# Kernel tuning notes

Measured on AMD Instinct MI355X. Metric: run time of the kernel, lower is better.

## Reference

```python
import jax, jax.numpy as jnp
import numpy as np

B, S, D, A = 8, 4096, 128, 128


def _pos_encoding(seq_len, dim):
    # sin/cos positional encoding, same construction as the torch buffer
    pos = np.arange(seq_len, dtype=np.float32)[:, None]
    div = np.exp(np.arange(0, dim, 2, dtype=np.float32) * (-np.log(10000.0) / dim))
    pe = np.zeros((seq_len, dim), dtype=np.float32)
    pe[:, 0::2] = np.sin(pos * div)
    pe[:, 1::2] = np.cos(pos * div)
    return jnp.asarray(pe)


def setup_inputs() -> dict:
    key = jax.random.key(0)
    ks = jax.random.split(key, 7)
    sc = 1.0 / np.sqrt(D)
    return {
        "x": jax.random.normal(ks[0], (B, S, D), dtype=jnp.float32),
        "Wq": jax.random.normal(ks[1], (D, A), dtype=jnp.float32) * sc,
        "bq": jnp.zeros((A,), dtype=jnp.float32),
        "Wk": jax.random.normal(ks[2], (D, A), dtype=jnp.float32) * sc,
        "bk": jnp.zeros((A,), dtype=jnp.float32),
        "Wv": jax.random.normal(ks[3], (D, A), dtype=jnp.float32) * sc,
        "bv": jnp.zeros((A,), dtype=jnp.float32),
    }


def reference(x, Wq, bq, Wk, bk, Wv, bv):
    b, s, d = x.shape
    pe = _pos_encoding(s, d)  # [S, D]
    xp = x + pe[None]  # broadcast add of positional encoding
    q = xp @ Wq + bq  # [B, S, A]
    k = xp @ Wk + bk
    v = xp @ Wv + bv
    scale = 1.0 / jnp.sqrt(jnp.asarray(Wq.shape[1], dtype=jnp.float32))
    scores = jnp.einsum("bsa,bta->bst", q, k) * scale  # [B, S, S]
    weights = jax.nn.softmax(scores, axis=-1)
    out = jnp.einsum("bst,bta->bsa", weights, v)  # [B, S, A]
    return out
```

## Files before the change

kernel.cpp:

```cpp
#include <hip/hip_runtime.h>

#define BB 8
#define SS 4096
#define DD 128

typedef __attribute__((ext_vector_type(8))) short v8s;
typedef __attribute__((ext_vector_type(4))) float v4f;
typedef __attribute__((ext_vector_type(16))) float v16f;

__device__ __forceinline__ unsigned short f2bf(float f) {
    unsigned int u = __float_as_uint(f);
    u += 0x7fffu + ((u >> 16) & 1u);
    return (unsigned short)(u >> 16);
}
__device__ __forceinline__ unsigned int pk_bf16(float a, float b) {
    unsigned int ua = __float_as_uint(a) + 0x8000u;
    unsigned int ub = __float_as_uint(b) + 0x8000u;
    return __builtin_amdgcn_perm(ub, ua, 0x07060302u);
}

#if !defined(__HIP_DEVICE_COMPILE__)
#define MFMA16(a, b, c) (c)
#define MFMA32(a, b, c) (c)
#define GLDS16(g, l)
#define WAITVM(n)
#define WAITLGKM()
#define BAR()
#else
#define MFMA16(a, b, c) __builtin_amdgcn_mfma_f32_16x16x32_bf16((a), (b), (c), 0, 0, 0)
#define MFMA32(a, b, c) __builtin_amdgcn_mfma_f32_32x32x16_bf16((a), (b), (c), 0, 0, 0)
#define GLDS16(g, l)                                                         \
    __builtin_amdgcn_global_load_lds(                                        \
        (const __attribute__((address_space(1))) unsigned int*)(g),          \
        (__attribute__((address_space(3))) unsigned int*)(l), 16, 0, 0)
#define WAITVM(n) asm volatile("s_waitcnt vmcnt(" #n ")" ::: "memory")
#define WAITLGKM() asm volatile("s_waitcnt lgkmcnt(0)" ::: "memory")
#define BAR()                                                                \
    do {                                                                     \
        asm volatile("" ::: "memory");                                       \
        __builtin_amdgcn_s_barrier();                                        \
        __builtin_amdgcn_sched_barrier(0);                                   \
        asm volatile("" ::: "memory");                                       \
    } while (0)
#endif

#if !defined(__HIP_DEVICE_COMPILE__)
#define EXP2F(x) exp2f(x)
#elif __has_builtin(__builtin_amdgcn_exp2f)
#define EXP2F(x) __builtin_amdgcn_exp2f(x)
#else
#define EXP2F(x) exp2f(x)
#endif

#define QSCALE 0.12751743f

__global__ __launch_bounds__(256) void prep_kernel(
    const float* __restrict__ Wq, const float* __restrict__ Wk,
    const float* __restrict__ Wv, unsigned short* __restrict__ Wt)
{
    int id = blockIdx.x * 256 + threadIdx.x;
    int w = id >> 14;
    int n = (id >> 7) & 127;
    int k = id & 127;
    const float* W = (w == 0) ? Wq : (w == 1) ? Wk : Wv;
    Wt[id] = f2bf(W[k * 128 + n]);
}

__global__ __launch_bounds__(256, 2) void proj_kernel(
    const float* __restrict__ x, const unsigned short* __restrict__ Wt,
    const float* __restrict__ bq, const float* __restrict__ bk,
    const float* __restrict__ bv,
    unsigned short* __restrict__ qo, unsigned short* __restrict__ ko,
    unsigned short* __restrict__ vF)
{
    __shared__ __attribute__((aligned(16))) unsigned short w_lds[128 * 136];
    __shared__ __attribute__((aligned(16))) unsigned short o_lds[9216];

    const int tid = threadIdx.x;
    const int wave = tid >> 6;
    const int lane = tid & 63;
    const int quad = lane >> 4;
    const int l15 = lane & 15;
    const int rbase = blockIdx.x * 64;

    const int flatrow = rbase + wave * 16 + l15;
    const int srow = flatrow & 4095;
    v8s af[4];
#pragma unroll
    for (int kc = 0; kc < 4; ++kc) {
        const int kbase = kc * 32 + quad * 8;
        const v4f* xp = (const v4f*)(x + (size_t)flatrow * DD + kbase);
        v4f x0 = xp[0], x1 = xp[1];
        float p[8];
#pragma unroll
        for (int j = 0; j < 8; j += 2) {
            float freq = __expf((float)(kbase + j) * -0.07195578415606394f);
            float arg = (float)srow * freq;
            p[j] = __sinf(arg);
            p[j + 1] = __cosf(arg);
        }
        v8s a;
#pragma unroll
        for (int j = 0; j < 4; ++j) a[j] = (short)f2bf(x0[j] + p[j]);
#pragma unroll
        for (int j = 0; j < 4; ++j) a[4 + j] = (short)f2bf(x1[j] + p[4 + j]);
        af[kc] = a;
    }

    const int quadp = ((quad & 1) << 1) | (quad >> 1);
    const int b0 = rbase >> 12, s0 = rbase & 4095;
    const size_t t0 = (size_t)b0 * 128 + (s0 >> 5);

#pragma unroll 1
    for (int m = 0; m < 3; ++m) {
        const float* bias = (m == 0) ? bq : (m == 1) ? bk : bv;
        __syncthreads();
        const unsigned short* Wp = Wt + (m << 14);
#pragma unroll
        for (int it = 0; it < 8; ++it) {
            int id = it * 256 + tid;
            int n = id >> 4, c8 = id & 15;
            *(v8s*)(w_lds + n * 136 + c8 * 8) = *(const v8s*)(Wp + n * 128 + c8 * 8);
        }
        __syncthreads();

#pragma unroll
        for (int nb = 0; nb < 8; ++nb) {
            const int col = nb * 16 + l15;
            v4f acc = {0.f, 0.f, 0.f, 0.f};
#pragma unroll
            for (int kc = 0; kc < 4; ++kc) {
                v8s bf = *(const v8s*)(w_lds + col * 136 + kc * 32 + quad * 8);
                acc = MFMA16(af[kc], bf, acc);
            }
            float bval = bias[col];
#pragma unroll
            for (int reg = 0; reg < 4; ++reg) {
                float val = acc[reg] + bval;
                if (m == 0) {
                    int lr = wave * 16 + quad * 4 + reg;
                    o_lds[lr * 136 + col] = f2bf(val * QSCALE);
                } else if (m == 1) {
                    int lr = wave * 16 + quad * 4 + reg;
                    o_lds[lr * 136 + col] = f2bf(val);
                } else {
                    int plr = wave * 16 + quadp * 4 + reg;
                    o_lds[col * 72 + plr] = f2bf(val);
                }
            }
        }
        __syncthreads();

        if (m <= 1) {
            unsigned short* outp = (m == 0) ? qo : ko;
#pragma unroll
            for (int it = 0; it < 4; ++it) {
                int id = it * 256 + tid;
                int r = id >> 4, c8 = id & 15;
                *(v8s*)(outp + (size_t)(rbase + r) * DD + c8 * 8) =
                    *(const v8s*)(o_lds + r * 136 + c8 * 8);
            }
        } else {
#pragma unroll
            for (int it = 0; it < 4; ++it) {
                int id = it * 256 + tid;
                int c = id >> 7, col = id & 127;
                *(v8s*)(vF + (((t0 + (c >> 2)) * 4 + (c & 3)) * 128 + col) * 8) =
                    *(const v8s*)(o_lds + col * 72 + c * 8);
            }
        }
    }
}

#define HKEYS 2048
#define NT 32
__global__ __launch_bounds__(512, 2) void flash_kernel(
    const unsigned short* __restrict__ qp,
    const unsigned short* __restrict__ kp,
    const unsigned short* __restrict__ vF,
    float* __restrict__ outp)
{
    __shared__ __attribute__((aligned(16))) unsigned short k_lds[2][2][8192];
    __shared__ float xl[8][32];

    const int tid = threadIdx.x;
    const int wave = tid >> 6;
    const int lane = tid & 63;
    const int hi = lane >> 5;
    const int l31 = lane & 31;
    const int half = wave >> 2;
    const int qs = wave & 3;
    const int wv = wave & 3;
    const int bid = blockIdx.x;
    const int b = bid & 7;
    const int qt = bid >> 3;
    const int qbase = qt * 128;

    const size_t qrow = (size_t)(b * SS + qbase + qs * 32 + l31) * DD;
    v8s qf[8];
#pragma unroll
    for (int kc = 0; kc < 8; ++kc)
        qf[kc] = *(const v8s*)(qp + qrow + kc * 16 + hi * 8);

    v16f o[4];
#pragma unroll
    for (int fg = 0; fg < 4; ++fg)
#pragma unroll
        for (int r = 0; r < 16; ++r) o[fg][r] = 0.f;
    float lp = 0.f;

    const int kro = half * 32768 + l31 * 256 + ((hi ^ (l31 & 15)) << 4);

    const int krow = wv * 4 + (lane >> 4);
    const unsigned short* ksrc =
        kp + ((size_t)(b * SS + half * HKEYS) + krow) * DD +
        (((lane & 15) ^ krow) << 3);
    unsigned short* kd0 = &k_lds[half][0][wv * 512];

    const size_t tbase = ((size_t)(b * 128 + half * 64)) * 4096;
    const unsigned short* vW = vF + tbase + hi * 1024 + l31 * 8;

    v8s X[8], Y[8];
    auto stage = [&](int p, int t) {
        unsigned short* kd = kd0 + p * 8192;
        const unsigned short* ks = ksrc + (size_t)t * 64 * DD;
#pragma unroll
        for (int it = 0; it < 4; ++it)
            GLDS16(ks + (size_t)it * 16 * DD, kd + it * 2048);
    };
    auto loadV = [&](v8s (&buf)[8], int u) {
        const unsigned short* p = vW + (size_t)u * 4096;
#pragma unroll
        for (int g = 0; g < 2; ++g)
#pragma unroll
            for (int fg = 0; fg < 4; ++fg)
                buf[g * 4 + fg] = *(const v8s*)(p + g * 2048 + fg * 256);
    };
    auto compute = [&](int p, int sub, const v8s (&buf)[8]) {
        const int ka = kro + p * 16384 + sub * 8192;
        v16f s;
#pragma unroll
        for (int r = 0; r < 16; ++r) s[r] = 0.f;
#pragma unroll
        for (int kc = 0; kc < 8; ++kc) {
            v8s af = *(const v8s*)((const char*)k_lds + (ka ^ (kc << 5)));
            s = MFMA32(af, qf[kc], s);
        }
        float e[16];
#pragma unroll
        for (int r = 0; r < 16; ++r) e[r] = EXP2F(s[r]);
        lp += (((e[0] + e[1]) + (e[2] + e[3])) + ((e[4] + e[5]) + (e[6] + e[7]))) +
              (((e[8] + e[9]) + (e[10] + e[11])) + ((e[12] + e[13]) + (e[14] + e[15])));
        union { v8s v[2]; unsigned int u[8]; } P;
#pragma unroll
        for (int g = 0; g < 2; ++g)
#pragma unroll
            for (int m = 0; m < 4; ++m)
                P.u[g * 4 + m] = pk_bf16(e[2 * m + 8 * g], e[2 * m + 8 * g + 1]);
#pragma unroll
        for (int g = 0; g < 2; ++g)
#pragma unroll
            for (int fg = 0; fg < 4; ++fg)
                o[fg] = MFMA32(P.v[g], buf[g * 4 + fg], o[fg]);
    };

    stage(0, 0);
    loadV(X, 0);
    loadV(Y, 1);
#pragma unroll 1
    for (int t = 0; t < NT; t += 2) {
        stage(1, t + 1);
        WAITVM(12);
        BAR();
        compute(0, 0, X);
        loadV(X, 2 * t + 2);
        WAITVM(12);
        compute(0, 1, Y);
        loadV(Y, 2 * t + 3);
        WAITLGKM();
        BAR();
        if (t + 2 < NT) {
            stage(0, t + 2);
            WAITVM(12);
        } else {
            WAITVM(8);
        }
        BAR();
        compute(1, 0, X);
        if (t + 2 < NT) {
            loadV(X, 2 * t + 4);
            WAITVM(12);
        } else {
            WAITVM(0);
        }
        compute(1, 1, Y);
        if (t + 2 < NT) loadV(Y, 2 * t + 5);
        WAITLGKM();
        BAR();
    }

    lp += __shfl_xor(lp, 32);
    if (hi == 0) xl[wave][l31] = lp;

    float* kf = (float*)&k_lds[0][0][0];

    auto putO = [&](float* base) {
#pragma unroll
        for (int fg = 0; fg < 4; ++fg) {
            v4f* bp = (v4f*)(base + fg * 1024 + lane * 16);
#pragma unroll
            for (int c = 0; c < 4; ++c) {
                v4f tv = {o[fg][c * 4 + 0], o[fg][c * 4 + 1],
                          o[fg][c * 4 + 2], o[fg][c * 4 + 3]};
                bp[c ^ (lane & 3)] = tv;
            }
        }
    };
    auto addO = [&](const float* base) {
#pragma unroll
        for (int fg = 0; fg < 4; ++fg) {
            const v4f* bp = (const v4f*)(base + fg * 1024 + lane * 16);
#pragma unroll
            for (int c = 0; c < 4; ++c) {
                v4f tv = bp[c ^ (lane & 3)];
#pragma unroll
                for (int j = 0; j < 4; ++j) o[fg][c * 4 + j] += tv[j];
            }
        }
    };

    if (half == 1) putO(kf + qs * 4096);
    __syncthreads();
    if (half == 0) {
        addO(kf + qs * 4096);
        float ir[16];
#pragma unroll
        for (int r = 0; r < 16; ++r) {
            int qr = (r & 3) + 8 * (r >> 2) + 4 * hi;
            ir[r] = 1.0f / (xl[qs][qr] + xl[4 + qs][qr]);
        }
#pragma unroll
        for (int fg = 0; fg < 4; ++fg)
#pragma unroll
            for (int r = 0; r < 16; ++r) {
                int qr = (r & 3) + 8 * (r >> 2) + 4 * hi;
                outp[(size_t)(b * SS + qbase + qs * 32 + qr) * DD +
                     fg * 32 + l31] = o[fg][r] * ir[r];
            }
    }
}

extern "C" void kernel_launch(void* const* d_in, const int* in_sizes, int n_in,
                              void* d_out, int out_size, void* d_ws, size_t ws_size,
                              hipStream_t stream)
{
    const float* x  = (const float*)d_in[0];
    const float* Wq = (const float*)d_in[1];
    const float* bq = (const float*)d_in[2];
    const float* Wk = (const float*)d_in[3];
    const float* bk = (const float*)d_in[4];
    const float* Wv = (const float*)d_in[5];
    const float* bv = (const float*)d_in[6];
    float* out = (float*)d_out;

    unsigned short* Wt = (unsigned short*)d_ws;
    unsigned short* q  = Wt + 49152;
    unsigned short* k  = q + (size_t)BB * SS * DD;
    unsigned short* vF = k + (size_t)BB * SS * DD;

    hipLaunchKernelGGL(prep_kernel, dim3(192), dim3(256), 0, stream,
                       Wq, Wk, Wv, Wt);
    hipLaunchKernelGGL(proj_kernel, dim3(BB * SS / 64), dim3(256), 0, stream,
                       x, Wt, bq, bk, bv, q, k, vF);
    hipLaunchKernelGGL(flash_kernel, dim3(BB * SS / 128), dim3(512), 0, stream,
                       q, k, vF, out);
}
```

Before: 167.9 us.

## Interleave two score tiles per iteration and restructure K/V prefetch pipeline

The main loop now handles one 64-key tile per iteration, computing both 32-key sub-tiles together. Their QK MFMAs, exp2 work and PV MFMAs are interleaved so the two independent chains overlap instead of running back to back. V loads for the next tile are issued after the PV MFMAs, and the vmcnt wait thresholds are retuned to match. The intent is more instruction-level parallelism and hidden MFMA latency. In exchange it holds two score accumulators live, raising register pressure, and it changes how far ahead V is prefetched.

```diff
diff --git a/kernel.cpp b/kernel.cpp
--- a/kernel.cpp
+++ b/kernel.cpp
@@ -236,65 +236,70 @@
             for (int fg = 0; fg < 4; ++fg)
                 buf[g * 4 + fg] = *(const v8s*)(p + g * 2048 + fg * 256);
     };
-    auto compute = [&](int p, int sub, const v8s (&buf)[8]) {
-        const int ka = kro + p * 16384 + sub * 8192;
-        v16f s;
-#pragma unroll
-        for (int r = 0; r < 16; ++r) s[r] = 0.f;
-#pragma unroll
-        for (int kc = 0; kc < 8; ++kc) {
-            v8s af = *(const v8s*)((const char*)k_lds + (ka ^ (kc << 5)));
-            s = MFMA32(af, qf[kc], s);
-        }
-        float e[16];
-#pragma unroll
-        for (int r = 0; r < 16; ++r) e[r] = EXP2F(s[r]);
-        lp += (((e[0] + e[1]) + (e[2] + e[3])) + ((e[4] + e[5]) + (e[6] + e[7]))) +
-              (((e[8] + e[9]) + (e[10] + e[11])) + ((e[12] + e[13]) + (e[14] + e[15])));
-        union { v8s v[2]; unsigned int u[8]; } P;
-#pragma unroll
-        for (int g = 0; g < 2; ++g)
-#pragma unroll
-            for (int m = 0; m < 4; ++m)
-                P.u[g * 4 + m] = pk_bf16(e[2 * m + 8 * g], e[2 * m + 8 * g + 1]);
-#pragma unroll
-        for (int g = 0; g < 2; ++g)
-#pragma unroll
-            for (int fg = 0; fg < 4; ++fg)
-                o[fg] = MFMA32(P.v[g], buf[g * 4 + fg], o[fg]);
-    };
 
     stage(0, 0);
     loadV(X, 0);
     loadV(Y, 1);
 #pragma unroll 1
-    for (int t = 0; t < NT; t += 2) {
-        stage(1, t + 1);
-        WAITVM(12);
+    for (int t = 0; t < NT; ++t) {
+        const int p = t & 1;
+        if (t + 1 < NT) {
+            stage(p ^ 1, t + 1);
+            WAITVM(20);
+        } else {
+            WAITVM(16);
+        }
         BAR();
-        compute(0, 0, X);
-        loadV(X, 2 * t + 2);
-        WAITVM(12);
-        compute(0, 1, Y);
-        loadV(Y, 2 * t + 3);
-        WAITLGKM();
-        BAR();
-        if (t + 2 < NT) {
-            stage(0, t + 2);
-            WAITVM(12);
-        } else {
-            WAITVM(8);
-        }
-        BAR();
-        compute(1, 0, X);
-        if (t + 2 < NT) {
-            loadV(X, 2 * t + 4);
-            WAITVM(12);
-        } else {
-            WAITVM(0);
-        }
-        compute(1, 1, Y);
-        if (t + 2 < NT) loadV(Y, 2 * t + 5);
+
+        const int ka0 = kro + p * 16384;
+        const int ka1 = ka0 + 8192;
+        v16f s0, s1;
+#pragma unroll
+        for (int r = 0; r < 16; ++r) { s0[r] = 0.f; s1[r] = 0.f; }
+#pragma unroll
+        for (int kc = 0; kc < 8; ++kc) {
+            v8s a0 = *(const v8s*)((const char*)k_lds + (ka0 ^ (kc << 5)));
+            v8s a1 = *(const v8s*)((const char*)k_lds + (ka1 ^ (kc << 5)));
+            s0 = MFMA32(a0, qf[kc], s0);
+            s1 = MFMA32(a1, qf[kc], s1);
+        }
+
+        float e0[16], e1[16];
+#pragma unroll
+        for (int r = 0; r < 16; ++r) e0[r] = EXP2F(s0[r]);
+#pragma unroll
+        for (int r = 0; r < 16; ++r) e1[r] = EXP2F(s1[r]);
+        lp += ((((e0[0] + e0[1]) + (e0[2] + e0[3])) +
+                ((e0[4] + e0[5]) + (e0[6] + e0[7]))) +
+               (((e0[8] + e0[9]) + (e0[10] + e0[11])) +
+                ((e0[12] + e0[13]) + (e0[14] + e0[15])))) +
+              ((((e1[0] + e1[1]) + (e1[2] + e1[3])) +
+                ((e1[4] + e1[5]) + (e1[6] + e1[7]))) +
+               (((e1[8] + e1[9]) + (e1[10] + e1[11])) +
+                ((e1[12] + e1[13]) + (e1[14] + e1[15]))));
+        union PU { v8s v[2]; unsigned int u[8]; } P0, P1;
+#pragma unroll
+        for (int g = 0; g < 2; ++g)
+#pragma unroll
+            for (int m = 0; m < 4; ++m) {
+                P0.u[g * 4 + m] = pk_bf16(e0[2 * m + 8 * g], e0[2 * m + 8 * g + 1]);
+                P1.u[g * 4 + m] = pk_bf16(e1[2 * m + 8 * g], e1[2 * m + 8 * g + 1]);
+            }
+
+        if (t + 1 < NT) { WAITVM(4); } else { WAITVM(0); }
+
+#pragma unroll
+        for (int g = 0; g < 2; ++g)
+#pragma unroll
+            for (int fg = 0; fg < 4; ++fg) {
+                o[fg] = MFMA32(P0.v[g], X[g * 4 + fg], o[fg]);
+                o[fg] = MFMA32(P1.v[g], Y[g * 4 + fg], o[fg]);
+            }
+
+        if (t + 1 < NT) {
+            loadV(X, 2 * t + 2);
+            loadV(Y, 2 * t + 3);
+        }
         WAITLGKM();
         BAR();
     }
```

Measured after the change: 176.6 us. +5.1%, slower.
